# Kernel tuning notes

Measured on AMD Instinct MI355X. Metric: run time of the kernel, lower is better.

Reference implementation:

```python
import jax, jax.numpy as jnp
import numpy as np

B, S, H = 4, 4096, 2048
NH = 16
HD = H // NH  # 128


def setup_inputs() -> dict:
    key = jax.random.key(0)
    ks = jax.random.split(key, 11)
    scale = 1.0 / np.sqrt(H)
    inp = {"hidden_states": jax.random.normal(ks[0], (B, S, H), dtype=jnp.float32)}
    names = ["q", "k", "v", "g", "o"]
    for i, n in enumerate(names):
        inp[f"W{n}"] = jax.random.uniform(ks[1 + i], (H, H), dtype=jnp.float32, minval=-scale, maxval=scale)
        inp[f"b{n}"] = jax.random.uniform(ks[6 + i], (H,), dtype=jnp.float32, minval=-scale, maxval=scale)
    return inp


def reference(hidden_states, Wq, bq, Wk, bk, Wv, bv, Wg, bg, Wo, bo):
    x = hidden_states
    b, s, _ = x.shape

    def heads(t):  # [b,s,H] -> [b,nh,s,hd]
        return t.reshape(b, s, NH, HD).transpose(0, 2, 1, 3)

    q = heads(x @ Wq + bq)
    k = heads(x @ Wk + bk)
    v = heads(x @ Wv + bv)
    g = heads(jax.nn.sigmoid(x @ Wg + bg))
    # kv state: [b,h,d,e]; small per-head outer-product sum over seq
    kv = jnp.einsum('bhsd,bhse->bhde', k, v)
    out = jnp.einsum('bhsd,bhde->bhse', q, kv)
    out = (out * g).transpose(0, 2, 1, 3).reshape(b, s, -1)
    return out @ Wo + bo
```

## Files before the change

kernel.cpp:

```cpp
#include <hip/hip_runtime.h>
#include <stdint.h>

typedef unsigned short u16;
typedef unsigned int   u32;
typedef __bf16 bf16x8 __attribute__((ext_vector_type(8)));
typedef float  f32x4  __attribute__((ext_vector_type(4)));
typedef u16    u16x8  __attribute__((ext_vector_type(8)));
typedef u16    u16x4  __attribute__((ext_vector_type(4)));

#define NB    4
#define NS    4096
#define NHID  2048
#define NHEAD 16
#define HDIM  128
#define NKT   32

__device__ __forceinline__ u16 f2bf(float f) {
  u32 u = __builtin_bit_cast(u32, f);
  u = (u + 0x7fffu + ((u >> 16) & 1u)) >> 16;
  return (u16)u;
}
__device__ __forceinline__ float bf2f(u16 h) {
  return __builtin_bit_cast(float, ((u32)h) << 16);
}

__device__ __forceinline__ void async_copy16(u16* lds_dst, const u16* g_src) {
  __builtin_amdgcn_global_load_lds(
      (__attribute__((address_space(1))) u32*)(const_cast<u16*>(g_src)),
      (__attribute__((address_space(3))) u32*)(lds_dst),
      16, 0, 0);
}

__device__ __forceinline__ void stage_half(u16* dst, const u16* src, int tid)
{
#pragma unroll
  for (int i = 0; i < 2; ++i) {
    const int u = (i << 9) + tid;
    const int r = u >> 2, gg = u & 3;
    const int col = ((gg ^ (r & 3)) << 3);
    async_copy16(dst + u * 8, src + (size_t)r * 2048 + col);
  }
}

template<int VM, int MH, int KH, bool SWAP>
__device__ __forceinline__ void phase8(const u16* Ac, const u16* Bc,
                                       bool stg, u16* sdst, const u16* ssrc,
                                       f32x4 (&acc)[8][4],
                                       int tid, int wr, int wc, int lr, int ggx)
{
  bf16x8 aR[4], bR[4];
#pragma unroll
  for (int m = 0; m < 4; ++m)
    aR[m] = *(const bf16x8*)(Ac + KH * 8192 + ((wr << 7) + MH * 64 + (m << 4) + lr) * 32 + ggx);
#pragma unroll
  for (int n = 0; n < 4; ++n)
    bR[n] = *(const bf16x8*)(Bc + KH * 8192 + ((wc << 6) + (n << 4) + lr) * 32 + ggx);

  if (stg) stage_half(sdst, ssrc, tid);

  if constexpr (VM >= 0) {
    asm volatile("s_waitcnt vmcnt(%0)" :: "n"(VM) : "memory");
  }
  __builtin_amdgcn_sched_barrier(0);
  __builtin_amdgcn_s_barrier();
  __builtin_amdgcn_sched_barrier(0);

  __builtin_amdgcn_s_setprio(1);
#pragma unroll
  for (int m = 0; m < 4; ++m)
#pragma unroll
    for (int n = 0; n < 4; ++n) {
      if (SWAP)
        acc[MH * 4 + m][n] = __builtin_amdgcn_mfma_f32_16x16x32_bf16(bR[n], aR[m], acc[MH * 4 + m][n], 0, 0, 0);
      else
        acc[MH * 4 + m][n] = __builtin_amdgcn_mfma_f32_16x16x32_bf16(aR[m], bR[n], acc[MH * 4 + m][n], 0, 0, 0);
    }
  __builtin_amdgcn_s_setprio(0);
}

template<bool SWAP>
__device__ __forceinline__ void gemm8(const u16* __restrict__ A,
                                      const u16* __restrict__ B,
                                      f32x4 (&acc)[8][4],
                                      u16 (*LA)[16384], u16 (*LB)[16384])
{
  const int tid = threadIdx.x, lane = tid & 63, w = tid >> 6;
  const int wr = w >> 2, wc = w & 3, lg = lane >> 4, lr = lane & 15;
  const int ggx = ((lg ^ (lr & 3)) << 3);

#pragma unroll
  for (int m = 0; m < 8; ++m)
#pragma unroll
    for (int n = 0; n < 4; ++n) acc[m][n] = f32x4{0.f, 0.f, 0.f, 0.f};

  stage_half(LA[0],        A,      tid);
  stage_half(LB[0],        B,      tid);
  stage_half(LA[0] + 8192, A + 32, tid);
  stage_half(LB[0] + 8192, B + 32, tid);
  asm volatile("s_waitcnt vmcnt(4)" ::: "memory");
  __builtin_amdgcn_sched_barrier(0);
  __builtin_amdgcn_s_barrier();
  __builtin_amdgcn_sched_barrier(0);

#pragma unroll 1
  for (int t = 0; t < NKT - 1; ++t) {
    const u16* Ac = LA[t & 1];
    const u16* Bc = LB[t & 1];
    u16* An = LA[(t + 1) & 1];
    u16* Bn = LB[(t + 1) & 1];
    const u16* As  = A + (t + 1) * 64;
    const u16* Bsr = B + (t + 1) * 64;
    phase8<-1, 0, 0, SWAP>(Ac, Bc, true, An,        As,       acc, tid, wr, wc, lr, ggx);
    phase8< 4, 1, 0, SWAP>(Ac, Bc, true, Bn,        Bsr,      acc, tid, wr, wc, lr, ggx);
    phase8<-1, 0, 1, SWAP>(Ac, Bc, true, An + 8192, As + 32,  acc, tid, wr, wc, lr, ggx);
    phase8< 4, 1, 1, SWAP>(Ac, Bc, true, Bn + 8192, Bsr + 32, acc, tid, wr, wc, lr, ggx);
  }
  {
    const u16* Ac = LA[(NKT - 1) & 1];
    const u16* Bc = LB[(NKT - 1) & 1];
    phase8<-1, 0, 0, SWAP>(Ac, Bc, false, nullptr, nullptr, acc, tid, wr, wc, lr, ggx);
    phase8< 0, 1, 0, SWAP>(Ac, Bc, false, nullptr, nullptr, acc, tid, wr, wc, lr, ggx);
    phase8<-1, 0, 1, SWAP>(Ac, Bc, false, nullptr, nullptr, acc, tid, wr, wc, lr, ggx);
    phase8<-1, 1, 1, SWAP>(Ac, Bc, false, nullptr, nullptr, acc, tid, wr, wc, lr, ggx);
  }
}

__global__ __launch_bounds__(512, 2) void k_gemm_qkvg(
    const u16* __restrict__ xb, const u16* __restrict__ WT,
    const float* __restrict__ bias,
    u16* __restrict__ q, u16* __restrict__ kT, u16* __restrict__ vT,
    u16* __restrict__ g)
{
  __shared__ u16 LA[2][16384];
  __shared__ u16 LB[2][16384];
  const int bid = blockIdx.x;
  const int grp = bid >> 8, r = bid & 255;
  const int mt = ((grp & 3) << 4) + (r & 15);
  const int nt = ((grp >> 2) << 4) + (r >> 4);
  const size_t bm0 = (size_t)mt << 8;
  const int    bn0 = nt << 8;
  const int nblk = bn0 >> 11;
  const int ocol0 = bn0 & 2047;

  const int tid = threadIdx.x, lane = tid & 63, w = tid >> 6;
  const int wr = w >> 2, wc = w & 3, lg = lane >> 4, lr = lane & 15;

  f32x4 acc[8][4];
  const u16* Ap = xb + bm0 * NHID;
  const u16* Bp = WT + (size_t)bn0 * NHID;

  if (nblk == 0 || nblk == 3) {
    gemm8<true>(Ap, Bp, acc, LA, LB);
    u16* outp = (nblk == 0) ? q : g;
    const bool sig = (nblk == 3);
#pragma unroll
    for (int m = 0; m < 8; ++m) {
      const size_t row = bm0 + (wr << 7) + (m << 4) + lr;
#pragma unroll
      for (int n = 0; n < 4; ++n) {
        const int colb = (wc << 6) + (n << 4) + (lg << 2);
        const float* bp = bias + bn0 + colb;
        u16x4 o;
#pragma unroll
        for (int j = 0; j < 4; ++j) {
          float val = acc[m][n][j] + bp[j];
          if (sig) val = 1.f / (1.f + __expf(-val));
          o[j] = f2bf(val);
        }
        *(u16x4*)(outp + row * NHID + ocol0 + colb) = o;
      }
    }
  } else {
    gemm8<false>(Ap, Bp, acc, LA, LB);
    u16* outp = (nblk == 1) ? kT : vT;
    const int b = (int)(bm0 >> 12);
    const int srow0 = (int)(bm0 & 4095) + (wr << 7) + (lg << 2);
#pragma unroll
    for (int m = 0; m < 8; ++m) {
      const int srow = srow0 + (m << 4);
#pragma unroll
      for (int n = 0; n < 4; ++n) {
        const int cg = ocol0 + (wc << 6) + (n << 4) + lr;
        const int h = cg >> 7, d = cg & 127;
        const float bia = bias[bn0 + (wc << 6) + (n << 4) + lr];
        u16x4 o;
#pragma unroll
        for (int j = 0; j < 4; ++j) o[j] = f2bf(acc[m][n][j] + bia);
        *(u16x4*)(outp + (((size_t)(b * NHEAD + h) * HDIM + d) << 12) + srow) = o;
      }
    }
  }
}

__global__ __launch_bounds__(512, 2) void k_gemm_out(
    const u16* __restrict__ attn, const u16* __restrict__ WoT,
    const float* __restrict__ bo, float* __restrict__ out)
{
  __shared__ u16 LA[2][16384];
  __shared__ u16 LB[2][16384];
  const int bid = blockIdx.x;
  const int grp = bid >> 7, rr = bid & 127;
  const int mt = (grp << 4) + (rr & 15);
  const int nt = rr >> 4;
  const size_t bm0 = (size_t)mt << 8;
  const int    bn0 = nt << 8;

  const int tid = threadIdx.x, lane = tid & 63, w = tid >> 6;
  const int wr = w >> 2, wc = w & 3, lg = lane >> 4, lr = lane & 15;

  f32x4 acc[8][4];
  gemm8<true>(attn + bm0 * NHID, WoT + (size_t)bn0 * NHID, acc, LA, LB);

#pragma unroll
  for (int m = 0; m < 8; ++m) {
    const size_t row = bm0 + (wr << 7) + (m << 4) + lr;
#pragma unroll
    for (int n = 0; n < 4; ++n) {
      const int colb = bn0 + (wc << 6) + (n << 4) + (lg << 2);
      f32x4 o;
#pragma unroll
      for (int j = 0; j < 4; ++j) o[j] = acc[m][n][j] + bo[colb + j];
      *(f32x4*)(out + row * NHID + colb) = o;
    }
  }
}

__device__ __forceinline__ void gemm_core(const u16* A, int lda,
                                          const u16* B, int ldb,
                                          int K, f32x4 acc[4][4],
                                          u16* As, u16* Bs)
{
  const int tid  = threadIdx.x;
  const int lane = tid & 63;
  const int w    = tid >> 6;
  const int wr   = (w >> 1) << 6;
  const int wc   = (w & 1) << 6;
  const int lg   = lane >> 4;
  const int lr   = lane & 15;

#pragma unroll
  for (int m = 0; m < 4; ++m)
#pragma unroll
    for (int n = 0; n < 4; ++n) acc[m][n] = f32x4{0.f, 0.f, 0.f, 0.f};

  for (int k0 = 0; k0 < K; k0 += 32) {
#pragma unroll
    for (int issue = 0; issue < 2; ++issue) {
      int c   = issue * 256 + tid;
      int row = c >> 2, cc = (c & 3) << 3;
      async_copy16(As + c * 8, A + (size_t)row * lda + k0 + cc);
    }
#pragma unroll
    for (int issue = 0; issue < 2; ++issue) {
      int c   = issue * 256 + tid;
      int row = c >> 2, cc = (c & 3) << 3;
      async_copy16(Bs + c * 8, B + (size_t)row * ldb + k0 + cc);
    }
    __syncthreads();

    bf16x8 af[4], bv[4];
#pragma unroll
    for (int m = 0; m < 4; ++m)
      af[m] = *(const bf16x8*)(As + ((wr + m * 16 + lr) << 5) + (lg << 3));
#pragma unroll
    for (int n = 0; n < 4; ++n)
      bv[n] = *(const bf16x8*)(Bs + ((wc + n * 16 + lr) << 5) + (lg << 3));

#pragma unroll
    for (int m = 0; m < 4; ++m)
#pragma unroll
      for (int n = 0; n < 4; ++n)
        acc[m][n] = __builtin_amdgcn_mfma_f32_16x16x32_bf16(af[m], bv[n], acc[m][n], 0, 0, 0);

    __syncthreads();
  }
}

__global__ __launch_bounds__(256) void k_gemm_kv(
    const u16* __restrict__ vT, const u16* __restrict__ kT, float* __restrict__ part)
{
  __shared__ u16 As[128 * 32];
  __shared__ u16 Bs[128 * 32];
  const int bh = blockIdx.x, sp = blockIdx.y;
  const u16* A  = vT + (size_t)bh * (HDIM * NS) + sp * 512;
  const u16* Bt = kT + (size_t)bh * (HDIM * NS) + sp * 512;
  f32x4 acc[4][4];
  gemm_core(A, NS, Bt, NS, 512, acc, As, Bs);

  float* outp = part + ((size_t)sp * 64 + bh) * 16384;
  const int tid = threadIdx.x, lane = tid & 63, w = tid >> 6;
  const int wr = (w >> 1) << 6, wc = (w & 1) << 6, lg = lane >> 4, lr = lane & 15;
#pragma unroll
  for (int m = 0; m < 4; ++m)
#pragma unroll
    for (int n = 0; n < 4; ++n) {
      const int col = wc + n * 16 + lr;
#pragma unroll
      for (int j = 0; j < 4; ++j) {
        const int row = wr + m * 16 + lg * 4 + j;
        outp[row * 128 + col] = acc[m][n][j];
      }
    }
}

__global__ __launch_bounds__(256) void k_gemm_attn(
    const u16* __restrict__ q, const u16* __restrict__ kvT,
    const u16* __restrict__ g, u16* __restrict__ attn)
{
  __shared__ u16 As[128 * 32];
  __shared__ u16 Bs[128 * 32];
  const int st = blockIdx.x, bh = blockIdx.y;
  const int b = bh >> 4, h = bh & 15;
  const size_t bs0 = (size_t)b * NS + st * 128;
  f32x4 acc[4][4];
  gemm_core(q + bs0 * NHID + h * HDIM, NHID, kvT + (size_t)bh * 16384, HDIM, HDIM, acc, As, Bs);

  const int tid = threadIdx.x, lane = tid & 63, w = tid >> 6;
  const int wr = (w >> 1) << 6, wc = (w & 1) << 6, lg = lane >> 4, lr = lane & 15;
#pragma unroll
  for (int m = 0; m < 4; ++m)
#pragma unroll
    for (int n = 0; n < 4; ++n) {
      const int col = wc + n * 16 + lr;
#pragma unroll
      for (int j = 0; j < 4; ++j) {
        const int row = wr + m * 16 + lg * 4 + j;
        const size_t idx = (bs0 + row) * NHID + h * HDIM + col;
        attn[idx] = f2bf(acc[m][n][j] * bf2f(g[idx]));
      }
    }
}

__global__ __launch_bounds__(256) void k_cvt_x(const float* __restrict__ x, u16* __restrict__ xb)
{
  const size_t i = (size_t)blockIdx.x * 256 + threadIdx.x;
  const float4* xf = (const float4*)x;
  float4 a = xf[2 * i];
  float4 b = xf[2 * i + 1];
  u16x8 o;
  o[0] = f2bf(a.x); o[1] = f2bf(a.y); o[2] = f2bf(a.z); o[3] = f2bf(a.w);
  o[4] = f2bf(b.x); o[5] = f2bf(b.y); o[6] = f2bf(b.z); o[7] = f2bf(b.w);
  ((u16x8*)xb)[i] = o;
}

__global__ __launch_bounds__(256) void k_cvt_w_t(const float* __restrict__ W, u16* __restrict__ WT)
{
  __shared__ u16 t[64][72];
  const int kt = blockIdx.x, nt = blockIdx.y;
  const int tid = threadIdx.x;
#pragma unroll
  for (int pass = 0; pass < 4; ++pass) {
    int c = pass * 256 + tid;
    int r = c >> 4, cc = (c & 15) << 2;
    float4 vv = *(const float4*)(W + (size_t)(kt * 64 + r) * 2048 + nt * 64 + cc);
    u16x4 o;
    o[0] = f2bf(vv.x); o[1] = f2bf(vv.y); o[2] = f2bf(vv.z); o[3] = f2bf(vv.w);
    *(u16x4*)&t[r][cc] = o;
  }
  __syncthreads();
#pragma unroll
  for (int pass = 0; pass < 2; ++pass) {
    int c = pass * 256 + tid;
    int rn = c >> 3, cs = (c & 7) << 3;
    u16x8 o;
#pragma unroll
    for (int j = 0; j < 8; ++j) o[j] = t[cs + j][rn];
    *(u16x8*)(WT + (size_t)(nt * 64 + rn) * 2048 + kt * 64 + cs) = o;
  }
}

__global__ __launch_bounds__(256) void k_bias_cat(
    const float* __restrict__ bq, const float* __restrict__ bk,
    const float* __restrict__ bv, const float* __restrict__ bg, float* __restrict__ o)
{
  const int i = blockIdx.x * 256 + threadIdx.x;
  const int blk = i >> 11;
  const float* s = (blk == 0) ? bq : (blk == 1) ? bk : (blk == 2) ? bv : bg;
  o[i] = s[i & 2047];
}

__global__ __launch_bounds__(256) void k_kv_reduce(const float* __restrict__ part, u16* __restrict__ kvT)
{
  const int i = blockIdx.x * 256 + threadIdx.x;
  float s = 0.f;
#pragma unroll
  for (int sp = 0; sp < 8; ++sp) s += part[(size_t)sp * 1048576 + i];
  kvT[i] = f2bf(s);
}

extern "C" void kernel_launch(void* const* d_in, const int* in_sizes, int n_in,
                              void* d_out, int out_size, void* d_ws, size_t ws_size,
                              hipStream_t stream)
{
  const float* x  = (const float*)d_in[0];
  const float* Wq = (const float*)d_in[1];
  const float* bq = (const float*)d_in[2];
  const float* Wk = (const float*)d_in[3];
  const float* bk = (const float*)d_in[4];
  const float* Wv = (const float*)d_in[5];
  const float* bv = (const float*)d_in[6];
  const float* Wg = (const float*)d_in[7];
  const float* bg = (const float*)d_in[8];
  const float* Wo = (const float*)d_in[9];
  const float* bo = (const float*)d_in[10];
  float* out = (float*)d_out;

  char* ws = (char*)d_ws;
  u16*   xb   = (u16*)(ws + 0x00000000ULL);
  u16*   WT   = (u16*)(ws + 0x04000000ULL);
  u16*   WoT  = (u16*)(ws + 0x06000000ULL);
  float* bias = (float*)(ws + 0x06800000ULL);
  u16*   q    = (u16*)(ws + 0x06900000ULL);
  u16*   kT   = (u16*)(ws + 0x0A900000ULL);
  u16*   vT   = (u16*)(ws + 0x0E900000ULL);
  u16*   gg   = (u16*)(ws + 0x12900000ULL);
  u16*   kvT  = (u16*)(ws + 0x16900000ULL);
  float* part = (float*)WT;
  u16*   attn = xb;

  if (ws_size < 0x16B00000ULL) return;

  k_cvt_x<<<16384, 256, 0, stream>>>(x, xb);
  k_cvt_w_t<<<dim3(32, 32), 256, 0, stream>>>(Wq, WT);
  k_cvt_w_t<<<dim3(32, 32), 256, 0, stream>>>(Wk, WT + (size_t)2048 * 2048);
  k_cvt_w_t<<<dim3(32, 32), 256, 0, stream>>>(Wv, WT + (size_t)2 * 2048 * 2048);
  k_cvt_w_t<<<dim3(32, 32), 256, 0, stream>>>(Wg, WT + (size_t)3 * 2048 * 2048);
  k_cvt_w_t<<<dim3(32, 32), 256, 0, stream>>>(Wo, WoT);
  k_bias_cat<<<32, 256, 0, stream>>>(bq, bk, bv, bg, bias);

  k_gemm_qkvg<<<2048, 512, 0, stream>>>(xb, WT, bias, q, kT, vT, gg);

  k_gemm_kv<<<dim3(64, 8), 256, 0, stream>>>(vT, kT, part);
  k_kv_reduce<<<4096, 256, 0, stream>>>(part, kvT);

  k_gemm_attn<<<dim3(32, 64), 256, 0, stream>>>(q, kvT, gg, attn);
  k_gemm_out<<<512, 512, 0, stream>>>(attn, WoT, bo, out);
}
```

Before: 892.6 us.

## Restructure GEMM mainloop with register-prefetched LDS fragments and row-split staging

```diff
diff --git a/kernel.cpp b/kernel.cpp
--- a/kernel.cpp
+++ b/kernel.cpp
@@ -31,97 +31,136 @@
       16, 0, 0);
 }
 
-__device__ __forceinline__ void stage_half(u16* dst, const u16* src, int tid)
+#define SBAR()  __builtin_amdgcn_sched_barrier(0)
+#define BARRIER() do { SBAR(); __builtin_amdgcn_s_barrier(); SBAR(); } while (0)
+#define LGKM0() asm volatile("s_waitcnt lgkmcnt(0)" ::: "memory")
+#define VM0()   asm volatile("s_waitcnt vmcnt(0)"   ::: "memory")
+
+__device__ __forceinline__ void stage9(u16* dst, const u16* src, int kt, int tid)
 {
 #pragma unroll
   for (int i = 0; i < 2; ++i) {
-    const int u = (i << 9) + tid;
-    const int r = u >> 2, gg = u & 3;
-    const int col = ((gg ^ (r & 3)) << 3);
-    async_copy16(dst + u * 8, src + (size_t)r * 2048 + col);
-  }
-}
-
-template<int VM, int MH, int KH, bool SWAP>
-__device__ __forceinline__ void phase8(const u16* Ac, const u16* Bc,
-                                       bool stg, u16* sdst, const u16* ssrc,
-                                       f32x4 (&acc)[8][4],
-                                       int tid, int wr, int wc, int lr, int ggx)
-{
-  bf16x8 aR[4], bR[4];
-#pragma unroll
-  for (int m = 0; m < 4; ++m)
-    aR[m] = *(const bf16x8*)(Ac + KH * 8192 + ((wr << 7) + MH * 64 + (m << 4) + lr) * 32 + ggx);
-#pragma unroll
-  for (int n = 0; n < 4; ++n)
-    bR[n] = *(const bf16x8*)(Bc + KH * 8192 + ((wc << 6) + (n << 4) + lr) * 32 + ggx);
-
-  if (stg) stage_half(sdst, ssrc, tid);
-
-  if constexpr (VM >= 0) {
-    asm volatile("s_waitcnt vmcnt(%0)" :: "n"(VM) : "memory");
-  }
-  __builtin_amdgcn_sched_barrier(0);
-  __builtin_amdgcn_s_barrier();
-  __builtin_amdgcn_sched_barrier(0);
-
+    const int U = (i << 9) + tid;
+    const int r = U >> 3, u = U & 7;
+    const int col = (kt << 6) + ((u ^ (r & 7)) << 3);
+    async_copy16(dst + U * 8, src + (size_t)r * 2048 + col);
+  }
+}
+
+__device__ __forceinline__ void rd_a(bf16x8 (&d)[4], const u16* base,
+                                     int kg, int mq, int lg, int lr)
+{
+#pragma unroll
+  for (int m = 0; m < 4; ++m) {
+    const int row = (mq << 6) + (m << 4) + lr;
+    const int c = ((kg << 2) | lg) ^ (row & 7);
+    d[m] = *(const bf16x8*)(base + row * 64 + (c << 3));
+  }
+}
+
+__device__ __forceinline__ void rd_b(bf16x8 (&d)[4], const u16* base,
+                                     int kg, int lg, int lr)
+{
+#pragma unroll
+  for (int n = 0; n < 4; ++n) {
+    const int row = (n << 4) + lr;
+    const int c = ((kg << 2) | lg) ^ (row & 7);
+    d[n] = *(const bf16x8*)(base + row * 64 + (c << 3));
+  }
+}
+
+template<bool SWAP>
+__device__ __forceinline__ void mmcl(f32x4 (&acc)[8][4], int mq,
+                                     const bf16x8 (&a)[4], const bf16x8 (&b)[4])
+{
   __builtin_amdgcn_s_setprio(1);
 #pragma unroll
-  for (int m = 0; m < 4; ++m)
+  for (int mm = 0; mm < 4; ++mm)
 #pragma unroll
     for (int n = 0; n < 4; ++n) {
       if (SWAP)
-        acc[MH * 4 + m][n] = __builtin_amdgcn_mfma_f32_16x16x32_bf16(bR[n], aR[m], acc[MH * 4 + m][n], 0, 0, 0);
+        acc[mq * 4 + mm][n] = __builtin_amdgcn_mfma_f32_16x16x32_bf16(b[n], a[mm], acc[mq * 4 + mm][n], 0, 0, 0);
       else
-        acc[MH * 4 + m][n] = __builtin_amdgcn_mfma_f32_16x16x32_bf16(aR[m], bR[n], acc[MH * 4 + m][n], 0, 0, 0);
+        acc[mq * 4 + mm][n] = __builtin_amdgcn_mfma_f32_16x16x32_bf16(a[mm], b[n], acc[mq * 4 + mm][n], 0, 0, 0);
     }
   __builtin_amdgcn_s_setprio(0);
 }
 
 template<bool SWAP>
-__device__ __forceinline__ void gemm8(const u16* __restrict__ A,
+__device__ __forceinline__ void gemm9(const u16* __restrict__ A,
                                       const u16* __restrict__ B,
-                                      f32x4 (&acc)[8][4],
-                                      u16 (*LA)[16384], u16 (*LB)[16384])
+                                      f32x4 (&acc)[8][4], u16* L)
 {
   const int tid = threadIdx.x, lane = tid & 63, w = tid >> 6;
   const int wr = w >> 2, wc = w & 3, lg = lane >> 4, lr = lane & 15;
-  const int ggx = ((lg ^ (lr & 3)) << 3);
 
 #pragma unroll
   for (int m = 0; m < 8; ++m)
 #pragma unroll
     for (int n = 0; n < 4; ++n) acc[m][n] = f32x4{0.f, 0.f, 0.f, 0.f};
 
-  stage_half(LA[0],        A,      tid);
-  stage_half(LB[0],        B,      tid);
-  stage_half(LA[0] + 8192, A + 32, tid);
-  stage_half(LB[0] + 8192, B + 32, tid);
-  asm volatile("s_waitcnt vmcnt(4)" ::: "memory");
-  __builtin_amdgcn_sched_barrier(0);
-  __builtin_amdgcn_s_barrier();
-  __builtin_amdgcn_sched_barrier(0);
+  const u16* A1 = A + (size_t)128 * 2048;
+  const u16* B1 = B + (size_t)128 * 2048;
+  const int aoff = wr * 8192;
+  const int boff = 16384 + ((wc >> 1) * 8192) + ((wc & 1) * 4096);
+
+  stage9(L,                 A,  0, tid);
+  stage9(L + 8192,          A1, 0, tid);
+  stage9(L + 16384,         B,  0, tid);
+  stage9(L + 16384 + 8192,  B1, 0, tid);
+  VM0();
+  BARRIER();
+
+  bf16x8 aRa[4], aRb[4], bR0[4], bR1[4];
+  rd_a(aRa, L + aoff, 0, 0, lg, lr);
+  rd_b(bR0, L + boff, 0, lg, lr);
+  LGKM0();
 
 #pragma unroll 1
   for (int t = 0; t < NKT - 1; ++t) {
-    const u16* Ac = LA[t & 1];
-    const u16* Bc = LB[t & 1];
-    u16* An = LA[(t + 1) & 1];
-    u16* Bn = LB[(t + 1) & 1];
-    const u16* As  = A + (t + 1) * 64;
-    const u16* Bsr = B + (t + 1) * 64;
-    phase8<-1, 0, 0, SWAP>(Ac, Bc, true, An,        As,       acc, tid, wr, wc, lr, ggx);
-    phase8< 4, 1, 0, SWAP>(Ac, Bc, true, Bn,        Bsr,      acc, tid, wr, wc, lr, ggx);
-    phase8<-1, 0, 1, SWAP>(Ac, Bc, true, An + 8192, As + 32,  acc, tid, wr, wc, lr, ggx);
-    phase8< 4, 1, 1, SWAP>(Ac, Bc, true, Bn + 8192, Bsr + 32, acc, tid, wr, wc, lr, ggx);
+    u16* Lc = L + ((t & 1) << 15);
+    u16* Ln = L + (((t + 1) & 1) << 15);
+    stage9(Ln,                A,  t + 1, tid);
+    stage9(Ln + 16384,        B,  t + 1, tid);
+    BARRIER();
+    rd_a(aRb, Lc + aoff, 0, 1, lg, lr);
+    mmcl<SWAP>(acc, 0, aRa, bR0);
+    LGKM0();
+    stage9(Ln + 8192,         A1, t + 1, tid);
+    stage9(Ln + 16384 + 8192, B1, t + 1, tid);
+    BARRIER();
+    rd_a(aRa, Lc + aoff, 1, 0, lg, lr);
+    rd_b(bR1, Lc + boff, 1, lg, lr);
+    mmcl<SWAP>(acc, 1, aRb, bR0);
+    LGKM0();
+    BARRIER();
+    rd_a(aRb, Lc + aoff, 1, 1, lg, lr);
+    mmcl<SWAP>(acc, 0, aRa, bR1);
+    LGKM0();
+    VM0();
+    BARRIER();
+    rd_a(aRa, Ln + aoff, 0, 0, lg, lr);
+    rd_b(bR0, Ln + boff, 0, lg, lr);
+    mmcl<SWAP>(acc, 1, aRb, bR1);
+    LGKM0();
   }
   {
-    const u16* Ac = LA[(NKT - 1) & 1];
-    const u16* Bc = LB[(NKT - 1) & 1];
-    phase8<-1, 0, 0, SWAP>(Ac, Bc, false, nullptr, nullptr, acc, tid, wr, wc, lr, ggx);
-    phase8< 0, 1, 0, SWAP>(Ac, Bc, false, nullptr, nullptr, acc, tid, wr, wc, lr, ggx);
-    phase8<-1, 0, 1, SWAP>(Ac, Bc, false, nullptr, nullptr, acc, tid, wr, wc, lr, ggx);
-    phase8<-1, 1, 1, SWAP>(Ac, Bc, false, nullptr, nullptr, acc, tid, wr, wc, lr, ggx);
+    u16* Lc = L + (((NKT - 1) & 1) << 15);
+    BARRIER();
+    rd_a(aRb, Lc + aoff, 0, 1, lg, lr);
+    mmcl<SWAP>(acc, 0, aRa, bR0);
+    LGKM0();
+    BARRIER();
+    rd_a(aRa, Lc + aoff, 1, 0, lg, lr);
+    rd_b(bR1, Lc + boff, 1, lg, lr);
+    mmcl<SWAP>(acc, 1, aRb, bR0);
+    LGKM0();
+    BARRIER();
+    rd_a(aRb, Lc + aoff, 1, 1, lg, lr);
+    mmcl<SWAP>(acc, 0, aRa, bR1);
+    LGKM0();
+    BARRIER();
+    mmcl<SWAP>(acc, 1, aRb, bR1);
   }
 }
 
@@ -131,8 +170,7 @@
     u16* __restrict__ q, u16* __restrict__ kT, u16* __restrict__ vT,
     u16* __restrict__ g)
 {
-  __shared__ u16 LA[2][16384];
-  __shared__ u16 LB[2][16384];
+  __shared__ u16 L[65536];
   const int bid = blockIdx.x;
   const int grp = bid >> 8, r = bid & 255;
   const int mt = ((grp & 3) << 4) + (r & 15);
@@ -150,7 +188,7 @@
   const u16* Bp = WT + (size_t)bn0 * NHID;
 
   if (nblk == 0 || nblk == 3) {
-    gemm8<true>(Ap, Bp, acc, LA, LB);
+    gemm9<true>(Ap, Bp, acc, L);
     u16* outp = (nblk == 0) ? q : g;
     const bool sig = (nblk == 3);
 #pragma unroll
@@ -171,7 +209,7 @@
       }
     }
   } else {
-    gemm8<false>(Ap, Bp, acc, LA, LB);
+    gemm9<false>(Ap, Bp, acc, L);
     u16* outp = (nblk == 1) ? kT : vT;
     const int b = (int)(bm0 >> 12);
     const int srow0 = (int)(bm0 & 4095) + (wr << 7) + (lg << 2);
@@ -196,8 +234,7 @@
     const u16* __restrict__ attn, const u16* __restrict__ WoT,
     const float* __restrict__ bo, float* __restrict__ out)
 {
-  __shared__ u16 LA[2][16384];
-  __shared__ u16 LB[2][16384];
+  __shared__ u16 L[65536];
   const int bid = blockIdx.x;
   const int grp = bid >> 7, rr = bid & 127;
   const int mt = (grp << 4) + (rr & 15);
@@ -209,7 +246,7 @@
   const int wr = w >> 2, wc = w & 3, lg = lane >> 4, lr = lane & 15;
 
   f32x4 acc[8][4];
-  gemm8<true>(attn + bm0 * NHID, WoT + (size_t)bn0 * NHID, acc, LA, LB);
+  gemm9<true>(attn + bm0 * NHID, WoT + (size_t)bn0 * NHID, acc, L);
 
 #pragma unroll
   for (int m = 0; m < 8; ++m) {
```

Measured after the change: 794.3 us. 1.12x faster.
